# Performance work log

Measured on AMD Instinct MI355X. Metric: run time of the kernel, lower is better.

## Reference

```python
import jax, jax.numpy as jnp
import numpy as np

# module hyper-parameters (VoronoiDecoder defaults)
S = 256          # n_seeds
Q = 262144       # query uv points
EPS = 1e-8
W_MIN = 0.005
BETA = 0.02
RAW_TEMP = 5.0
H_MIN, H_MAX = 0.5, 2.0
J_BETA_SCALE = 1.0
J_WIDTH_BONUS = 0.15
J_KEFF_K0 = 3.0
J_KEFF_S = 0.35
J_TRIPLE_LAMBDA = 0.15
J_TRIPLE_POWER = 1.5
KNN_K = 8
SOFTMIN_TAU = 0.002


def setup_inputs() -> dict:
    key = jax.random.key(0)
    ks = jax.random.split(key, 7)
    return {
        "uv": jax.random.uniform(ks[0], (Q, 2), jnp.float32),
        "seeds_raw": jax.random.uniform(ks[1], (S, 2), jnp.float32),
        "w_raw": jax.random.normal(ks[2], (S, S), jnp.float32),
        "h_raw": jax.random.normal(ks[3], (S,), jnp.float32),
        "theta": jax.random.normal(ks[4], (S,), jnp.float32),
        "a_raw": 0.3 * jax.random.normal(ks[5], (S,), jnp.float32),
        "seed_gates": jax.random.normal(ks[6], (S,), jnp.float32),
    }


def reference(uv, seeds_raw, w_raw, h_raw, theta, a_raw, seed_gates):
    seeds = seeds_raw  # seeds_uv is identity

    # --- pairwise seed distances (default buffers: all faces non-periodic,
    # seed_face_id all zero -> periodic wrap is a no-op -> plain euclidean) ---
    pd = jnp.linalg.norm(seeds[None, :, :] - seeds[:, None, :], axis=-1)  # (S,S)
    w_max_pair = jnp.maximum(0.8 * pd, W_MIN + EPS)
    w_geo = W_MIN + (w_max_pair - W_MIN) * jax.nn.sigmoid(w_raw / RAW_TEMP)
    W = 0.5 * (w_geo + w_geo.T)  # symmetric pairwise wall widths (S,S)

    h = H_MIN + (H_MAX - H_MIN) * jax.nn.sigmoid(h_raw)  # (S,) heights
    gates = jax.nn.sigmoid(seed_gates)                    # (S,) seed gates

    # --- anisotropic (unit-determinant) metric distance per seed ---
    c, sn = jnp.cos(theta), jnp.sin(theta)
    sc = jnp.exp(a_raw)  # anisotropy scale per seed
    dx = uv[:, None, 0] - seeds[None, :, 0]  # (Q,S)
    dy = uv[:, None, 1] - seeds[None, :, 1]
    xp = (c * dx + sn * dy) / sc   # rotate into seed frame, scale axes
    yp = (-sn * dx + c * dy) * sc
    d = jnp.sqrt(xp * xp + yp * yp + EPS)  # (Q,S) metric distances

    # --- kNN over seeds ---
    negk, idx = jax.lax.top_k(-d, KNN_K)   # (Q,K)
    dk = -negk
    d1, d3 = dk[:, 0], dk[:, 2]
    i1, i2 = idx[:, 0], idx[:, 1]
    w_pair = W[i1, i2]  # width of the wall between the 2 nearest cells

    # --- junction effects via softmin cell-membership weights ---
    p = jax.nn.softmax(-d / (BETA * J_BETA_SCALE), axis=-1)  # (Q,S)
    k_eff = 1.0 / (jnp.sum(p * p, axis=-1) + EPS)            # effective #cells
    bonus = J_WIDTH_BONUS * jax.nn.sigmoid((k_eff - J_KEFF_K0) / J_KEFF_S)
    triple = J_TRIPLE_LAMBDA * jnp.exp(-((d3 - d1) / (w_pair + EPS)) ** J_TRIPLE_POWER)
    w_eff = w_pair * (1.0 + bonus + triple)

    # --- softmin distance to Voronoi boundary over kNN bisectors ---
    b = 0.5 * (dk[:, 1:] - d1[:, None])  # (Q,K-1) bisector half-gaps
    sdist = -SOFTMIN_TAU * jax.nn.logsumexp(-b / SOFTMIN_TAU, axis=-1)
    wall = jax.nn.sigmoid((0.5 * w_eff - sdist) / BETA)  # shell occupancy

    h_blend = p @ h        # (Q,) blended height
    g_blend = p @ gates    # (Q,) blended gate
    return wall * g_blend * h_blend
```

## Files before the change

### kernel.cpp

```cpp
#include <hip/hip_runtime.h>

#define NSEED 256
#define HALF_STRIDE 1040

typedef float v2f __attribute__((ext_vector_type(2)));
typedef float v4f __attribute__((ext_vector_type(4)));

__device__ __forceinline__ float fast_exp(float x) {
  return __builtin_amdgcn_exp2f(x * 1.4426950408889634f);
}
__device__ __forceinline__ float sigf(float x) {
  return 1.0f / (1.0f + fast_exp(-x));
}
__device__ __forceinline__ float med3(float x, float lo, float hi) {
  return __builtin_amdgcn_fmed3f(x, lo, hi);
}
__device__ __forceinline__ v2f vfma(v2f a, v2f b, v2f c) {
  return __builtin_elementwise_fma(a, b, c);
}

__global__ __launch_bounds__(256) void voronoi_kernel(
    const float* __restrict__ uv, const float* __restrict__ seeds,
    const float* __restrict__ w_raw, const float* __restrict__ h_raw,
    const float* __restrict__ theta, const float* __restrict__ a_raw,
    const float* __restrict__ seed_gates, float* __restrict__ out, int nq) {
  __shared__ float Ppf[2 * HALF_STRIDE];

  {
    int s = threadIdx.x;
    float sx = seeds[2 * s], sy = seeds[2 * s + 1];
    float th = theta[s];
    float c = cosf(th), sn = sinf(th);
    float sc = expf(a_raw[s]);
    float inv = 1.0f / sc;
    float h = 0.5f + 1.5f * sigf(h_raw[s]);
    float g = sigf(seed_gates[s]);
    int pair = s >> 1, b = s & 1;
    int half = pair >> 6, lp = pair & 63;
    float* base = Ppf + half * HALF_STRIDE + lp * 16;
    base[0 + b] = sx;
    base[2 + b] = sy;
    base[4 + b] = c * inv;
    base[6 + b] = sn * inv;
    base[8 + b] = -sn * sc;
    base[10 + b] = c * sc;
    base[12 + b] = h;
    base[14 + b] = g;
  }
  __syncthreads();

  const int t = blockIdx.x * 256 + threadIdx.x;
  const int q = t >> 1;
  const int par = t & 1;
  if (q >= nq) return;
  const float2 uvq = ((const float2*)uv)[q];
  const v2f uu = {uvq.x, uvq.x}, vv = {uvq.y, uvq.y};
  const v2f eps2 = {1e-8f, 1e-8f};
  const float NK = -72.13475204444817f;

  float dk0 = 3e38f, dk1 = 3e38f, dk2 = 3e38f, dk3 = 3e38f;
  float dk4 = 3e38f, dk5 = 3e38f, dk6 = 3e38f, dk7 = 3e38f;
  int i0 = 0, i1 = 0;
  v2f S1 = {0.f, 0.f}, S2 = {0.f, 0.f}, Sh = {0.f, 0.f}, Sg = {0.f, 0.f};

#define INS(x, sidx)             \
  {                              \
    float _d = (x);              \
    bool c0 = _d < dk0;          \
    bool c1 = _d < dk1;          \
    int sh = c0 ? i0 : (sidx);   \
    i1 = c1 ? sh : i1;           \
    i0 = c0 ? (sidx) : i0;       \
    dk7 = med3(_d, dk6, dk7);    \
    dk6 = med3(_d, dk5, dk6);    \
    dk5 = med3(_d, dk4, dk5);    \
    dk4 = med3(_d, dk3, dk4);    \
    dk3 = med3(_d, dk2, dk3);    \
    dk2 = med3(_d, dk1, dk2);    \
    dk1 = med3(_d, dk0, dk1);    \
    dk0 = fminf(_d, dk0);        \
  }

  const v4f* __restrict__ PF = (const v4f*)(Ppf + par * HALF_STRIDE);
#pragma unroll 8
  for (int k = 0; k < 64; ++k) {
    v4f q0 = PF[4 * k + 0];
    v4f q1 = PF[4 * k + 1];
    v4f q2 = PF[4 * k + 2];
    v4f q3 = PF[4 * k + 3];
    v2f dx = uu - q0.xy, dy = vv - q0.zw;
    v2f xp = vfma(q1.xy, dx, q1.zw * dy);
    v2f yp = vfma(q2.xy, dx, q2.zw * dy);
    v2f d2 = vfma(xp, xp, vfma(yp, yp, eps2));
    INS(d2.x, 2 * k);
    INS(d2.y, 2 * k + 1);
    float da = __builtin_amdgcn_sqrtf(d2.x);
    float db = __builtin_amdgcn_sqrtf(d2.y);
    v2f e;
    e.x = __builtin_amdgcn_exp2f(da * NK);
    e.y = __builtin_amdgcn_exp2f(db * NK);
    S1 += e;
    S2 = vfma(e, e, S2);
    Sh = vfma(e, q3.xy, Sh);
    Sg = vfma(e, q3.zw, Sg);
  }
#undef INS

  i0 |= par << 7;
  i1 |= par << 7;

  float b0 = __shfl_xor(dk0, 1), b1 = __shfl_xor(dk1, 1);
  float b2 = __shfl_xor(dk2, 1), b3 = __shfl_xor(dk3, 1);
  float b4 = __shfl_xor(dk4, 1), b5 = __shfl_xor(dk5, 1);
  float b6 = __shfl_xor(dk6, 1), b7 = __shfl_xor(dk7, 1);
  int j0 = __shfl_xor(i0, 1), j1 = __shfl_xor(i1, 1);
  bool aw = b0 < dk0;
  int I0 = aw ? j0 : i0;
  float ec1 = aw ? dk0 : dk1;
  int ic1 = aw ? i0 : i1;
  float ec2 = aw ? b1 : b0;
  int ic2 = aw ? j1 : j0;
  int I1 = (ec2 < ec1) ? ic2 : ic1;

  float m0 = fminf(dk0, b7), m1 = fminf(dk1, b6);
  float m2 = fminf(dk2, b5), m3 = fminf(dk3, b4);
  float m4 = fminf(dk4, b3), m5 = fminf(dk5, b2);
  float m6 = fminf(dk6, b1), m7 = fminf(dk7, b0);
#define CE(a, b)             \
  {                          \
    float _lo = fminf(a, b); \
    float _hi = fmaxf(a, b); \
    a = _lo;                 \
    b = _hi;                 \
  }
  CE(m0, m4) CE(m1, m5) CE(m2, m6) CE(m3, m7)
  CE(m0, m2) CE(m1, m3) CE(m4, m6) CE(m5, m7)
  CE(m0, m1) CE(m2, m3) CE(m4, m5) CE(m6, m7)
#undef CE

  dk0 = __builtin_amdgcn_sqrtf(m0);
  dk1 = __builtin_amdgcn_sqrtf(m1);
  dk2 = __builtin_amdgcn_sqrtf(m2);
  dk3 = __builtin_amdgcn_sqrtf(m3);
  dk4 = __builtin_amdgcn_sqrtf(m4);
  dk5 = __builtin_amdgcn_sqrtf(m5);
  dk6 = __builtin_amdgcn_sqrtf(m6);
  dk7 = __builtin_amdgcn_sqrtf(m7);
  const float d1 = dk0, d3 = dk2;

  float S1s = S1.x + S1.y;
  float S2s = S2.x + S2.y;
  float Shs = Sh.x + Sh.y;
  float Sgs = Sg.x + Sg.y;
  S1s += __shfl_xor(S1s, 1);
  S2s += __shfl_xor(S2s, 1);
  Shs += __shfl_xor(Shs, 1);
  Sgs += __shfl_xor(Sgs, 1);

  float ax = seeds[2 * I0], ay = seeds[2 * I0 + 1];
  float bx = seeds[2 * I1], by = seeds[2 * I1 + 1];
  float pdx = ax - bx, pdy = ay - by;
  float pd = __builtin_amdgcn_sqrtf(fmaf(pdx, pdx, pdy * pdy));
  float wmax = fmaxf(0.8f * pd, 0.005f + 1e-8f);
  float wr01 = w_raw[(I0 << 8) + I1];
  float wr10 = w_raw[(I1 << 8) + I0];
  float w_pair = 0.005f + (wmax - 0.005f) * 0.5f * (sigf(wr01 * 0.2f) + sigf(wr10 * 0.2f));

  float s1sq = S1s * S1s;
  float keff = s1sq / fmaf(1e-8f, s1sq, S2s);
  float bonus = 0.15f * sigf((keff - 3.0f) * (1.0f / 0.35f));

  float tt = (d3 - d1) / (w_pair + 1e-8f);
  float t15 = tt * __builtin_amdgcn_sqrtf(tt);
  float triple = 0.15f * fast_exp(-t15);

  float w_eff = w_pair * (1.0f + bonus + triple);

  const float HT = 360.6737602222409f;
  float acc = 1.0f;
  acc += __builtin_amdgcn_exp2f((dk1 - dk2) * HT);
  acc += __builtin_amdgcn_exp2f((dk1 - dk3) * HT);
  acc += __builtin_amdgcn_exp2f((dk1 - dk4) * HT);
  acc += __builtin_amdgcn_exp2f((dk1 - dk5) * HT);
  acc += __builtin_amdgcn_exp2f((dk1 - dk6) * HT);
  acc += __builtin_amdgcn_exp2f((dk1 - dk7) * HT);
  float b1s = 0.5f * (dk1 - d1);
  float sdist = b1s - 0.002f * 0.6931471805599453f * __builtin_amdgcn_logf(acc);

  float wall = sigf((0.5f * w_eff - sdist) * 50.0f);
  float invS1 = 1.0f / S1s;
  if (par == 0) out[q] = wall * (Sgs * invS1) * (Shs * invS1);
}

extern "C" void kernel_launch(void* const* d_in, const int* in_sizes, int n_in,
                              void* d_out, int out_size, void* d_ws, size_t ws_size,
                              hipStream_t stream) {
  (void)in_sizes;
  (void)n_in;
  (void)d_ws;
  (void)ws_size;
  const float* uv = (const float*)d_in[0];
  const float* seeds = (const float*)d_in[1];
  const float* w_raw = (const float*)d_in[2];
  const float* h_raw = (const float*)d_in[3];
  const float* theta = (const float*)d_in[4];
  const float* a_raw = (const float*)d_in[5];
  const float* gates = (const float*)d_in[6];
  float* out = (float*)d_out;

  int nq = out_size;
  long long threads = 2LL * nq;
  int grid = (int)((threads + 255) / 256);
  voronoi_kernel<<<grid, 256, 0, stream>>>(uv, seeds, w_raw, h_raw, theta,
                                           a_raw, gates, out, nq);
}
```

Before: 115.0 us.

## Split each query's seed scan across four lanes and software-prefetch LDS

Each query is now handled by four threads, each scanning 64 seeds, where before two threads each scanned 128. The per-lane top-8 lists and index pairs are merged through a two-stage butterfly of shuffles, and the partial sums are reduced across four lanes. The LDS loads for the next seed pair are issued one iteration ahead to hide latency. This shortens the serial per-thread chain and adds parallelism, at the cost of twice as many threads, an extra merge and shuffle stage, and four-times-redundant epilogue work for every stored output.

```diff
diff --git a/kernel.cpp b/kernel.cpp
--- a/kernel.cpp
+++ b/kernel.cpp
@@ -1,7 +1,7 @@
 #include <hip/hip_runtime.h>
 
 #define NSEED 256
-#define HALF_STRIDE 1040
+#define QSTRIDE 520
 
 typedef float v2f __attribute__((ext_vector_type(2)));
 typedef float v4f __attribute__((ext_vector_type(4)));
@@ -24,7 +24,7 @@
     const float* __restrict__ w_raw, const float* __restrict__ h_raw,
     const float* __restrict__ theta, const float* __restrict__ a_raw,
     const float* __restrict__ seed_gates, float* __restrict__ out, int nq) {
-  __shared__ float Ppf[2 * HALF_STRIDE];
+  __shared__ float Ppf[4 * QSTRIDE + 16];
 
   {
     int s = threadIdx.x;
@@ -35,9 +35,8 @@
     float inv = 1.0f / sc;
     float h = 0.5f + 1.5f * sigf(h_raw[s]);
     float g = sigf(seed_gates[s]);
-    int pair = s >> 1, b = s & 1;
-    int half = pair >> 6, lp = pair & 63;
-    float* base = Ppf + half * HALF_STRIDE + lp * 16;
+    int quarter = s >> 6, lp = (s >> 1) & 31, b = s & 1;
+    float* base = Ppf + quarter * QSTRIDE + lp * 16;
     base[0 + b] = sx;
     base[2 + b] = sy;
     base[4 + b] = c * inv;
@@ -50,8 +49,8 @@
   __syncthreads();
 
   const int t = blockIdx.x * 256 + threadIdx.x;
-  const int q = t >> 1;
-  const int par = t & 1;
+  const int q = t >> 2;
+  const int par = t & 3;
   if (q >= nq) return;
   const float2 uvq = ((const float2*)uv)[q];
   const v2f uu = {uvq.x, uvq.x}, vv = {uvq.y, uvq.y};
@@ -81,13 +80,14 @@
     dk0 = fminf(_d, dk0);        \
   }
 
-  const v4f* __restrict__ PF = (const v4f*)(Ppf + par * HALF_STRIDE);
+  const v4f* __restrict__ PF = (const v4f*)(Ppf + par * QSTRIDE);
+  v4f q0 = PF[0], q1 = PF[1], q2 = PF[2], q3 = PF[3];
 #pragma unroll 8
-  for (int k = 0; k < 64; ++k) {
-    v4f q0 = PF[4 * k + 0];
-    v4f q1 = PF[4 * k + 1];
-    v4f q2 = PF[4 * k + 2];
-    v4f q3 = PF[4 * k + 3];
+  for (int k = 0; k < 32; ++k) {
+    v4f n0 = PF[4 * k + 4];
+    v4f n1 = PF[4 * k + 5];
+    v4f n2 = PF[4 * k + 6];
+    v4f n3 = PF[4 * k + 7];
     v2f dx = uu - q0.xy, dy = vv - q0.zw;
     v2f xp = vfma(q1.xy, dx, q1.zw * dy);
     v2f yp = vfma(q2.xy, dx, q2.zw * dy);
@@ -103,29 +103,13 @@
     S2 = vfma(e, e, S2);
     Sh = vfma(e, q3.xy, Sh);
     Sg = vfma(e, q3.zw, Sg);
+    q0 = n0; q1 = n1; q2 = n2; q3 = n3;
   }
 #undef INS
 
-  i0 |= par << 7;
-  i1 |= par << 7;
-
-  float b0 = __shfl_xor(dk0, 1), b1 = __shfl_xor(dk1, 1);
-  float b2 = __shfl_xor(dk2, 1), b3 = __shfl_xor(dk3, 1);
-  float b4 = __shfl_xor(dk4, 1), b5 = __shfl_xor(dk5, 1);
-  float b6 = __shfl_xor(dk6, 1), b7 = __shfl_xor(dk7, 1);
-  int j0 = __shfl_xor(i0, 1), j1 = __shfl_xor(i1, 1);
-  bool aw = b0 < dk0;
-  int I0 = aw ? j0 : i0;
-  float ec1 = aw ? dk0 : dk1;
-  int ic1 = aw ? i0 : i1;
-  float ec2 = aw ? b1 : b0;
-  int ic2 = aw ? j1 : j0;
-  int I1 = (ec2 < ec1) ? ic2 : ic1;
-
-  float m0 = fminf(dk0, b7), m1 = fminf(dk1, b6);
-  float m2 = fminf(dk2, b5), m3 = fminf(dk3, b4);
-  float m4 = fminf(dk4, b3), m5 = fminf(dk5, b2);
-  float m6 = fminf(dk6, b1), m7 = fminf(dk7, b0);
+  i0 |= par << 6;
+  i1 |= par << 6;
+
 #define CE(a, b)             \
   {                          \
     float _lo = fminf(a, b); \
@@ -133,19 +117,44 @@
     a = _lo;                 \
     b = _hi;                 \
   }
-  CE(m0, m4) CE(m1, m5) CE(m2, m6) CE(m3, m7)
-  CE(m0, m2) CE(m1, m3) CE(m4, m6) CE(m5, m7)
-  CE(m0, m1) CE(m2, m3) CE(m4, m5) CE(m6, m7)
+#define MERGE(W)                                                     \
+  {                                                                  \
+    float b0 = __shfl_xor(dk0, W), b1 = __shfl_xor(dk1, W);          \
+    float b2 = __shfl_xor(dk2, W), b3 = __shfl_xor(dk3, W);          \
+    float b4 = __shfl_xor(dk4, W), b5 = __shfl_xor(dk5, W);          \
+    float b6 = __shfl_xor(dk6, W), b7 = __shfl_xor(dk7, W);          \
+    int j0 = __shfl_xor(i0, W), j1 = __shfl_xor(i1, W);              \
+    bool aw = b0 < dk0;                 \
+    float ec1 = aw ? dk0 : dk1;                                      \
+    int ic1 = aw ? i0 : i1;                                          \
+    float ec2 = aw ? b1 : b0;                                        \
+    int ic2 = aw ? j1 : j0;                                          \
+    i0 = aw ? j0 : i0;                                               \
+    i1 = (ec2 < ec1) ? ic2 : ic1;                                    \
+    float m0 = fminf(dk0, b7), m1 = fminf(dk1, b6);                  \
+    float m2 = fminf(dk2, b5), m3 = fminf(dk3, b4);                  \
+    float m4 = fminf(dk4, b3), m5 = fminf(dk5, b2);                  \
+    float m6 = fminf(dk6, b1), m7 = fminf(dk7, b0);                  \
+    CE(m0, m4) CE(m1, m5) CE(m2, m6) CE(m3, m7)                      \
+    CE(m0, m2) CE(m1, m3) CE(m4, m6) CE(m5, m7)                      \
+    CE(m0, m1) CE(m2, m3) CE(m4, m5) CE(m6, m7)                      \
+    dk0 = m0; dk1 = m1; dk2 = m2; dk3 = m3;                          \
+    dk4 = m4; dk5 = m5; dk6 = m6; dk7 = m7;                          \
+  }
+  MERGE(1)
+  MERGE(2)
+#undef MERGE
 #undef CE
 
-  dk0 = __builtin_amdgcn_sqrtf(m0);
-  dk1 = __builtin_amdgcn_sqrtf(m1);
-  dk2 = __builtin_amdgcn_sqrtf(m2);
-  dk3 = __builtin_amdgcn_sqrtf(m3);
-  dk4 = __builtin_amdgcn_sqrtf(m4);
-  dk5 = __builtin_amdgcn_sqrtf(m5);
-  dk6 = __builtin_amdgcn_sqrtf(m6);
-  dk7 = __builtin_amdgcn_sqrtf(m7);
+  const int I0 = i0, I1 = i1;
+  dk0 = __builtin_amdgcn_sqrtf(dk0);
+  dk1 = __builtin_amdgcn_sqrtf(dk1);
+  dk2 = __builtin_amdgcn_sqrtf(dk2);
+  dk3 = __builtin_amdgcn_sqrtf(dk3);
+  dk4 = __builtin_amdgcn_sqrtf(dk4);
+  dk5 = __builtin_amdgcn_sqrtf(dk5);
+  dk6 = __builtin_amdgcn_sqrtf(dk6);
+  dk7 = __builtin_amdgcn_sqrtf(dk7);
   const float d1 = dk0, d3 = dk2;
 
   float S1s = S1.x + S1.y;
@@ -156,6 +165,10 @@
   S2s += __shfl_xor(S2s, 1);
   Shs += __shfl_xor(Shs, 1);
   Sgs += __shfl_xor(Sgs, 1);
+  S1s += __shfl_xor(S1s, 2);
+  S2s += __shfl_xor(S2s, 2);
+  Shs += __shfl_xor(Shs, 2);
+  Sgs += __shfl_xor(Sgs, 2);
 
   float ax = seeds[2 * I0], ay = seeds[2 * I0 + 1];
   float bx = seeds[2 * I1], by = seeds[2 * I1 + 1];
@@ -209,7 +222,7 @@
   float* out = (float*)d_out;
 
   int nq = out_size;
-  long long threads = 2LL * nq;
+  long long threads = 4LL * nq;
   int grid = (int)((threads + 255) / 256);
   voronoi_kernel<<<grid, 256, 0, stream>>>(uv, seeds, w_raw, h_raw, theta,
                                            a_raw, gates, out, nq);
```

Result: slower. 119.7 us (+4.1%).
